# Optimization experiments

Hardware: AMD Instinct MI355X
Metric: run time of the kernel (lower is better)

The kernel has to match this reference:

```python
import jax, jax.numpy as jnp
import numpy as np

# ---- static config (mirrors Net.__init__) ----
N_NODES, N_EDGES = 4000, 20000
N_PROTS, D = 919, 512            # node_emb: Embedding(919, 512); F_in = D (divide_input=False)
TOWERS, F_OUT = 4, D // 4        # F_out = out_channels // towers = 128
EDGE_D = 50
N_GRAPHS, N_CLASSES = 32, 10
N_LAYERS = 2
EPS_BN, EPS_STD = 1e-5, 1e-5

# deg histogram passed to PNAConv; only avg_deg['log'] matters for the scalers used
DEG_HIST = np.array([0., 800., 1200., 900., 600., 300., 150., 50.])
AVG_DEG_LOG = float((np.log(np.arange(DEG_HIST.size) + 1.0) * DEG_HIST).sum() / DEG_HIST.sum())


def setup_inputs() -> dict:
    key = jax.random.key(0)
    ks = jax.random.split(key, 16)
    g = lambda i, shape, s=0.05: (jax.random.normal(ks[i], shape, jnp.float32) * s)
    return dict(
        node_emb_w=g(0, (N_PROTS, D), 0.1),
        edge_emb_w=g(1, (2, EDGE_D), 0.1),
        pe_w=g(2, (2, D)), pe_b=jnp.zeros((D,), jnp.float32),
        edge_enc_w=g(3, (N_LAYERS, EDGE_D, D)), edge_enc_b=jnp.zeros((N_LAYERS, D), jnp.float32),
        pre_w=g(4, (N_LAYERS, TOWERS, 3 * D, D)), pre_b=jnp.zeros((N_LAYERS, TOWERS, D), jnp.float32),
        post_w=g(5, (N_LAYERS, TOWERS, 13 * D, F_OUT)), post_b=jnp.zeros((N_LAYERS, TOWERS, F_OUT), jnp.float32),
        lin_w=g(6, (N_LAYERS, D, D)), lin_b=jnp.zeros((N_LAYERS, D), jnp.float32),
        bn_gamma=jnp.ones((N_LAYERS, D), jnp.float32), bn_beta=jnp.zeros((N_LAYERS, D), jnp.float32),
        acts=jax.random.normal(ks[7], (N_NODES, 2), jnp.float32),
        fc1_w=g(8, (D, 2 * D)), fc1_b=jnp.zeros((2 * D,), jnp.float32),
        fc_out_w=g(9, (2 * D, N_CLASSES)), fc_out_b=jnp.zeros((N_CLASSES,), jnp.float32),
        prelu_a=jnp.float32(0.25),
        global_idx=jax.random.randint(ks[10], (N_NODES,), 0, N_PROTS),
        sign=jax.random.randint(ks[11], (N_EDGES,), 0, 2),
        edge_index=jax.random.randint(ks[12], (2, N_EDGES), 0, N_NODES),
        batch=jnp.sort(jax.random.randint(ks[13], (N_NODES,), 0, N_GRAPHS)),
    )


def _pna_layer(x, src, dst, e, pre_w, pre_b, post_w, post_b, lin_w, lin_b):
    # x: [N, D], e: [E, D] (edge_encoder output), pre_w: [T, 3D, D], post_w: [T, 13D, F_OUT]
    N, E = x.shape[0], src.shape[0]
    # pre-NN on cat([x_i, x_j, edge_attr]) expressed as split matmuls (pre_layers=1 -> single Linear)
    Wi, Wj, We = pre_w[:, :D], pre_w[:, D:2 * D], pre_w[:, 2 * D:]
    m = (jnp.einsum('ef,tfd->etd', x[dst], Wi)
         + jnp.einsum('ef,tfd->etd', x[src], Wj)
         + jnp.einsum('ef,tfd->etd', e, We) + pre_b)          # [E, T, D]
    # multi-aggregation at destination nodes: mean / min / max / std
    cnt = jax.ops.segment_sum(jnp.ones((E,), m.dtype), dst, N)  # in-degree
    has = (cnt > 0)[:, None, None]
    deg = jnp.maximum(cnt, 1.0)[:, None, None]                  # clamp(1) as in PyG
    s1 = jax.ops.segment_sum(m, dst, N)
    s2 = jax.ops.segment_sum(m * m, dst, N)
    mean = s1 / deg
    std = jnp.sqrt(jax.nn.relu(s2 / deg - mean * mean) + EPS_STD)
    mn = jnp.where(has, jax.ops.segment_min(m, dst, N), 0.0)
    mx = jnp.where(has, jax.ops.segment_max(m, dst, N), 0.0)
    agg = jnp.concatenate([mean, mn, mx, std], axis=-1)         # [N, T, 4D]
    # degree scalers: identity, amplification, attenuation
    amp = jnp.log(deg + 1.0) / AVG_DEG_LOG
    out = jnp.concatenate([agg, agg * amp, agg / amp], axis=-1)  # [N, T, 12D]
    # post-NN on cat([x, out]) as split matmuls (post_layers=1)
    Wx, Wo = post_w[:, :D], post_w[:, D:]
    o = (jnp.einsum('nf,tfd->ntd', x, Wx)
         + jnp.einsum('ntf,tfd->ntd', out, Wo) + post_b)        # [N, T, F_OUT]
    return o.reshape(N, TOWERS * F_OUT) @ lin_w + lin_b         # [N, D]


def reference(node_emb_w, edge_emb_w, pe_w, pe_b, edge_enc_w, edge_enc_b,
              pre_w, pre_b, post_w, post_b, lin_w, lin_b, bn_gamma, bn_beta,
              acts, fc1_w, fc1_b, fc_out_w, fc_out_b, prelu_a,
              global_idx, sign, edge_index, batch):
    src, dst = edge_index[0], edge_index[1]
    x = node_emb_w[global_idx] + (acts @ pe_w + pe_b)           # node_emb + PostEncoding
    ea = edge_emb_w[sign]                                       # [E, 50]
    for l in range(N_LAYERS):
        e = ea @ edge_enc_w[l] + edge_enc_b[l]                  # shared edge encoder
        h = _pna_layer(x, src, dst, e, pre_w[l], pre_b[l], post_w[l], post_b[l], lin_w[l], lin_b[l])
        mu = h.mean(axis=0)
        var = ((h - mu) ** 2).mean(axis=0)                      # training-mode BatchNorm (biased var)
        x = jax.nn.relu(bn_gamma[l] * (h - mu) * jax.lax.rsqrt(var + EPS_BN) + bn_beta[l])
    pooled = jax.ops.segment_sum(x, batch, N_GRAPHS)            # global_add_pool
    z = pooled @ fc1_w + fc1_b
    z = jnp.where(z > 0, z, prelu_a * z)                        # PReLU
    logits = z @ fc_out_w + fc_out_b
    return jax.nn.log_softmax(logits, axis=-1)
```

## Files before the change

### kernel.cpp

```cpp
#include <hip/hip_runtime.h>
#include <hip/hip_bf16.h>
#include <float.h>

#define NN 4000
#define NE 20000
#define DD 512
#define NT 4
#define FO 128
#define NG 32
#define NC 10
#define XGW 4608
#define AVGLOG 1.2548916493836102f
#define EPS_STD_ 1e-5f
#define EPS_BN_ 1e-5f

typedef __bf16 bf16x8 __attribute__((ext_vector_type(8)));
typedef float  f32x4  __attribute__((ext_vector_type(4)));

__device__ __forceinline__ void async_copy16(const void* g, void* l) {
    __builtin_amdgcn_global_load_lds((const __attribute__((address_space(1))) void*)g,
                                     (__attribute__((address_space(3))) void*)l, 16, 0, 0);
}

__device__ __forceinline__ void mfma_core128(
    const __bf16* __restrict__ A, int lda,
    const __bf16* __restrict__ BT, int ldbt,
    __bf16* __restrict__ C, int ldc,
    int M, int K, int m0, int n0)
{
    __shared__ __bf16 As[128 * 32];
    __shared__ __bf16 Bs[128 * 32];
    const int tid = threadIdx.x;
    const int wave = tid >> 6, lane = tid & 63;
    const int wm = (wave >> 1) * 64, wn = (wave & 1) * 64;
    const int fr = lane & 15, fq = lane >> 4;
    const int fk = fq * 8;
    const int srow = lane >> 2;
    const int skc = (lane & 3) * 8;

    f32x4 acc[4][4];
    const f32x4 zero = {0.f, 0.f, 0.f, 0.f};
#pragma unroll
    for (int i = 0; i < 4; ++i)
#pragma unroll
        for (int j = 0; j < 4; ++j) acc[i][j] = zero;

    for (int k0 = 0; k0 < K; k0 += 32) {
#pragma unroll
        for (int q = 0; q < 2; ++q) {
            const int row = wave * 32 + q * 16 + srow;
            int ar = m0 + row; if (ar > M - 1) ar = M - 1;
            async_copy16(A + (size_t)ar * lda + k0 + skc, As + wave * 1024 + q * 512);
            async_copy16(BT + (size_t)(n0 + row) * ldbt + k0 + skc, Bs + wave * 1024 + q * 512);
        }
        __syncthreads();
        bf16x8 af[4], bfr[4];
#pragma unroll
        for (int mi = 0; mi < 4; ++mi) af[mi]  = *(const bf16x8*)(As + (wm + mi * 16 + fr) * 32 + fk);
#pragma unroll
        for (int ni = 0; ni < 4; ++ni) bfr[ni] = *(const bf16x8*)(Bs + (wn + ni * 16 + fr) * 32 + fk);
#pragma unroll
        for (int mi = 0; mi < 4; ++mi)
#pragma unroll
            for (int ni = 0; ni < 4; ++ni)
                acc[mi][ni] = __builtin_amdgcn_mfma_f32_16x16x32_bf16(af[mi], bfr[ni], acc[mi][ni], 0, 0, 0);
        __syncthreads();
    }
#pragma unroll
    for (int mi = 0; mi < 4; ++mi) {
#pragma unroll
        for (int ni = 0; ni < 4; ++ni) {
            const int col = n0 + wn + ni * 16 + fr;
            const int rb = m0 + wm + mi * 16 + fq * 4;
#pragma unroll
            for (int r = 0; r < 4; ++r) {
                const int rowc = rb + r;
                if (rowc < M) C[(size_t)rowc * ldc + col] = (__bf16)acc[mi][ni][r];
            }
        }
    }
}

__global__ __launch_bounds__(256) void k_xg(const __bf16* __restrict__ XB, const __bf16* __restrict__ WCAT,
                                            __bf16* __restrict__ XG) {
    mfma_core128(XB, 512, WCAT, 512, XG, XGW, NN, 512, blockIdx.y * 128, blockIdx.x * 128);
}

__global__ __launch_bounds__(256) void k_gw(const __bf16* __restrict__ AB, const __bf16* __restrict__ WTT,
                                            const __bf16* __restrict__ XG,
                                            const float* __restrict__ amp, const float* __restrict__ ramp,
                                            const float* __restrict__ pb, __bf16* __restrict__ OB,
                                            float* __restrict__ BN, float* __restrict__ PL, int zero_pl) {
    const int t = blockIdx.y;
    const int n0 = blockIdx.x * 32;
    __shared__ __bf16 As[32 * 32];
    __shared__ __bf16 Bs[384 * 32];
    __shared__ float  Ep[32][388];
    const int tid = threadIdx.x;
    const int wave = tid >> 6, lane = tid & 63;
    const int fr = lane & 15, fq = lane >> 4;
    const int wn = wave * 96;

    f32x4 acc[2][6];
    const f32x4 zero = {0.f, 0.f, 0.f, 0.f};
#pragma unroll
    for (int i = 0; i < 2; ++i)
#pragma unroll
        for (int j = 0; j < 6; ++j) acc[i][j] = zero;

    const __bf16* Abase = AB + (size_t)n0 * 8192 + (size_t)t * 2048;
    const __bf16* Bbase = WTT + (size_t)t * 384 * 2048;
    const int ar = tid >> 2, akc = (tid & 3) * 8;

    for (int k0 = 0; k0 < 2048; k0 += 32) {
        if (wave < 2)
            async_copy16(Abase + (size_t)ar * 8192 + k0 + akc, As + tid * 8);
#pragma unroll
        for (int i = 0; i < 6; ++i) {
            const int cb = tid + 256 * i;
            const int br = cb >> 2, bkc = (cb & 3) * 8;
            async_copy16(Bbase + (size_t)br * 2048 + k0 + bkc, Bs + cb * 8);
        }
        __syncthreads();
        bf16x8 a[2], b[6];
#pragma unroll
        for (int mi = 0; mi < 2; ++mi) a[mi] = *(const bf16x8*)(As + (mi * 16 + fr) * 32 + fq * 8);
#pragma unroll
        for (int ni = 0; ni < 6; ++ni) b[ni] = *(const bf16x8*)(Bs + (wn + ni * 16 + fr) * 32 + fq * 8);
#pragma unroll
        for (int mi = 0; mi < 2; ++mi)
#pragma unroll
            for (int ni = 0; ni < 6; ++ni)
                acc[mi][ni] = __builtin_amdgcn_mfma_f32_16x16x32_bf16(a[mi], b[ni], acc[mi][ni], 0, 0, 0);
        __syncthreads();
    }
#pragma unroll
    for (int mi = 0; mi < 2; ++mi)
#pragma unroll
        for (int ni = 0; ni < 6; ++ni)
#pragma unroll
            for (int r = 0; r < 4; ++r)
                Ep[mi * 16 + fq * 4 + r][wn + ni * 16 + fr] = acc[mi][ni][r];
    __syncthreads();
    const int row = tid >> 3, o0 = (tid & 7) * 16;
    const int n = n0 + row;
    const float av = amp[n], rv = ramp[n];
    bf16x8 gx0 = *(const bf16x8*)(XG + (size_t)n * XGW + 4096 + t * 128 + o0);
    bf16x8 gx1 = *(const bf16x8*)(XG + (size_t)n * XGW + 4096 + t * 128 + o0 + 8);
    bf16x8 ov0, ov1;
#pragma unroll
    for (int u = 0; u < 8; ++u) {
        int o = o0 + u;
        float v = (float)gx0[u] + Ep[row][o] + av * Ep[row][128 + o] + rv * Ep[row][256 + o] + pb[t * 128 + o];
        ov0[u] = (__bf16)v;
    }
#pragma unroll
    for (int u = 0; u < 8; ++u) {
        int o = o0 + 8 + u;
        float v = (float)gx1[u] + Ep[row][o] + av * Ep[row][128 + o] + rv * Ep[row][256 + o] + pb[t * 128 + o];
        ov1[u] = (__bf16)v;
    }
    *(bf16x8*)(OB + (size_t)n * 512 + t * 128 + o0) = ov0;
    *(bf16x8*)(OB + (size_t)n * 512 + t * 128 + o0 + 8) = ov1;
    if (blockIdx.x == 0 && blockIdx.y == 0) {
        BN[tid] = 0.f; BN[256 + tid] = 0.f; BN[512 + tid] = 0.f; BN[768 + tid] = 0.f;
        if (zero_pl)
            for (int i = tid; i < NG * DD; i += 256) PL[i] = 0.f;
    }
}

__global__ __launch_bounds__(256) void k_lin(const __bf16* __restrict__ OB, const __bf16* __restrict__ WLINT,
                                             const float* __restrict__ bl, float* __restrict__ H,
                                             float* __restrict__ BN) {
    const int n0c = blockIdx.x * 128, m0 = blockIdx.y * 64;
    __shared__ __bf16 As[64 * 32];
    __shared__ __bf16 Bs[128 * 32];
    __shared__ float bnS[128], bnQ[128];
    const int tid = threadIdx.x;
    if (tid < 128) { bnS[tid] = 0.f; bnQ[tid] = 0.f; }
    const int wave = tid >> 6, lane = tid & 63;
    const int wr = wave >> 1, wc = wave & 1;
    const int fr = lane & 15, fq = lane >> 4;
    f32x4 acc[2][4];
    const f32x4 zero = {0.f, 0.f, 0.f, 0.f};
#pragma unroll
    for (int i = 0; i < 2; ++i)
#pragma unroll
        for (int j = 0; j < 4; ++j) acc[i][j] = zero;

    const int ar = tid >> 2, akc = (tid & 3) * 8;
    int arow = m0 + ar; if (arow > NN - 1) arow = NN - 1;
    for (int k0 = 0; k0 < 512; k0 += 32) {
        async_copy16(OB + (size_t)arow * 512 + k0 + akc, As + tid * 8);
#pragma unroll
        for (int i = 0; i < 2; ++i) {
            const int cb = tid + 256 * i;
            const int br = cb >> 2, bkc = (cb & 3) * 8;
            async_copy16(WLINT + (size_t)(n0c + br) * 512 + k0 + bkc, Bs + cb * 8);
        }
        __syncthreads();
        bf16x8 a[2], b[4];
#pragma unroll
        for (int mi = 0; mi < 2; ++mi) a[mi] = *(const bf16x8*)(As + (wr * 32 + mi * 16 + fr) * 32 + fq * 8);
#pragma unroll
        for (int ni = 0; ni < 4; ++ni) b[ni] = *(const bf16x8*)(Bs + (wc * 64 + ni * 16 + fr) * 32 + fq * 8);
#pragma unroll
        for (int mi = 0; mi < 2; ++mi)
#pragma unroll
            for (int ni = 0; ni < 4; ++ni)
                acc[mi][ni] = __builtin_amdgcn_mfma_f32_16x16x32_bf16(a[mi], b[ni], acc[mi][ni], 0, 0, 0);
        __syncthreads();
    }
#pragma unroll
    for (int ni = 0; ni < 4; ++ni) {
        const int lc = wc * 64 + ni * 16 + fr;
        const int col = n0c + lc;
        const float bv = bl[col];
        float s = 0.f, q = 0.f;
#pragma unroll
        for (int mi = 0; mi < 2; ++mi) {
#pragma unroll
            for (int r = 0; r < 4; ++r) {
                const int rowc = m0 + wr * 32 + mi * 16 + fq * 4 + r;
                if (rowc < NN) {
                    const float v = acc[mi][ni][r] + bv;
                    H[(size_t)rowc * 512 + col] = v;
                    s += v; q += v * v;
                }
            }
        }
        atomicAdd(&bnS[lc], s); atomicAdd(&bnQ[lc], q);
    }
    __syncthreads();
    if (tid < 128) {
        atomicAdd(&BN[n0c + tid], bnS[tid]);
        atomicAdd(&BN[512 + n0c + tid], bnQ[tid]);
    }
}

__device__ __forceinline__ void tr32(const float* __restrict__ S, int sld,
                                     __bf16* __restrict__ D, int dld) {
    __shared__ float t[32][33];
    const int x = threadIdx.x, y0 = threadIdx.y * 4;
#pragma unroll
    for (int i = 0; i < 4; ++i) t[y0 + i][x] = S[(size_t)(y0 + i) * sld + x];
    __syncthreads();
#pragma unroll
    for (int i = 0; i < 4; ++i) D[(size_t)(y0 + i) * dld + x] = (__bf16)t[x][y0 + i];
}

__global__ void k_tr(const float* __restrict__ pw, const float* __restrict__ pow_,
                     const float* __restrict__ lw,
                     __bf16* __restrict__ WCAT, __bf16* __restrict__ WTT, __bf16* __restrict__ WLINT) {
    int id = blockIdx.x;
    if (id < 2048) {
        const int z = id >> 8, r = id & 255;
        const int t = z & 3, half = z >> 2;
        const int x = r & 15, y = r >> 4;
        const float* S = pw + ((size_t)(t * 1536 + half * 512 + y * 32)) * 512 + x * 32;
        __bf16* D = WCAT + ((size_t)(half * 2048 + t * 512 + x * 32)) * 512 + y * 32;
        tr32(S, 512, D, 512);
    } else if (id < 2304) {
        const int id3 = id - 2048;
        const int t = id3 >> 6, r = id3 & 63;
        const int x = r & 3, y = r >> 2;
        const float* S = pow_ + ((size_t)(t * 6656 + y * 32)) * 128 + x * 32;
        __bf16* D = WCAT + ((size_t)(4096 + t * 128 + x * 32)) * 512 + y * 32;
        tr32(S, 128, D, 512);
    } else if (id < 5376) {
        const int id4 = id - 2304;
        const int z = id4 >> 8, r = id4 & 255;
        const int t = z / 3, w = z % 3;
        const int x = r & 3, y = r >> 2;
        const float* S = pow_ + ((size_t)(t * 6656 + 512 + w * 2048 + y * 32)) * 128 + x * 32;
        __bf16* D = WTT + (size_t)t * 384 * 2048 + ((size_t)(w * 128 + x * 32)) * 2048 + y * 32;
        tr32(S, 128, D, 2048);
    } else {
        const int r = id - 5376;
        const int x = r & 15, y = r >> 4;
        const float* S = lw + (size_t)y * 32 * 512 + x * 32;
        __bf16* D = WLINT + (size_t)x * 32 * 512 + y * 32;
        tr32(S, 512, D, 512);
    }
}

__global__ void k_count(const int* __restrict__ dst, int* __restrict__ cnt) {
    int e = blockIdx.x * 256 + threadIdx.x;
    if (e < NE) atomicAdd(&cnt[dst[e]], 1);
}

__global__ __launch_bounds__(1024) void k_scan_bx(const int* __restrict__ cnt, int* __restrict__ offs,
                                                  float* __restrict__ amp, float* __restrict__ ramp,
                                                  const float* __restrict__ nemb, const float* __restrict__ acts,
                                                  const float* __restrict__ pew, const float* __restrict__ peb,
                                                  const int* __restrict__ gidx, __bf16* __restrict__ XB) {
    const int t = threadIdx.x;
    if (blockIdx.x == 0) {
        __shared__ int part[1024];
        const int base = t * 4;
        int loc[4]; int s = 0;
#pragma unroll
        for (int i = 0; i < 4; ++i) { int v = (base + i < NN) ? cnt[base + i] : 0; loc[i] = s; s += v; }
        part[t] = s;
        __syncthreads();
        for (int o = 1; o < 1024; o <<= 1) {
            int v = (t >= o) ? part[t - o] : 0;
            __syncthreads();
            part[t] += v;
            __syncthreads();
        }
        const int pre = (t > 0) ? part[t - 1] : 0;
#pragma unroll
        for (int i = 0; i < 4; ++i) if (base + i < NN) offs[base + i] = pre + loc[i];
        if (t == 1023) offs[NN] = part[1023];
        for (int n = t; n < NN; n += 1024) {
            float deg = fmaxf((float)cnt[n], 1.0f);
            float a = logf(deg + 1.0f) / AVGLOG;
            amp[n] = a; ramp[n] = 1.0f / a;
        }
    } else {
        const int idx = (blockIdx.x - 1) * 1024 + t;
        const int n = idx >> 9, d = idx & 511;
        float v = nemb[(size_t)gidx[n] * DD + d] + acts[n * 2] * pew[d] + acts[n * 2 + 1] * pew[DD + d] + peb[d];
        XB[idx] = (__bf16)v;
    }
}

__global__ void k_fill(const int* __restrict__ src, const int* __restrict__ dst,
                       const int* __restrict__ sgn, const int* __restrict__ offs,
                       int* __restrict__ fill, int* __restrict__ esrc, int* __restrict__ esgn) {
    int e = blockIdx.x * 256 + threadIdx.x;
    if (e < NE) {
        int d = dst[e];
        int pos = offs[d] + atomicAdd(&fill[d], 1);
        esrc[pos] = src[e];
        esgn[pos] = sgn[e];
    }
}

__global__ __launch_bounds__(256) void k_em(const float* __restrict__ eemb, const float* __restrict__ eew,
                                            const float* __restrict__ eeb, const float* __restrict__ pw,
                                            const float* __restrict__ pb, float* __restrict__ EM) {
    __shared__ float eks[512];
    __shared__ float part[4][64];
    const int tid = threadIdx.x;
    const int k = blockIdx.x >> 5;
    const int g0 = (blockIdx.x & 31) * 64;
#pragma unroll
    for (int h = 0; h < 2; ++h) {
        const int f = tid + h * 256;
        float s = eeb[f];
        for (int c = 0; c < 50; ++c) s += eemb[k * 50 + c] * eew[(size_t)c * 512 + f];
        eks[f] = s;
    }
    __syncthreads();
    const int wave = tid >> 6, lane = tid & 63;
    const int g = g0 + lane;
    const int t = g >> 9, d = g & 511;
    const float* Wp = pw + ((size_t)(t * 1536 + 1024)) * 512 + d;
    float s = 0.f;
    const int f0 = wave * 128;
#pragma unroll 4
    for (int f = f0; f < f0 + 128; ++f) s += eks[f] * Wp[(size_t)f * 512];
    part[wave][lane] = s;
    __syncthreads();
    if (tid < 64) {
        const int gg = g0 + tid;
        EM[k * 2048 + gg] = pb[gg] + part[0][tid] + part[1][tid] + part[2][tid] + part[3][tid];
    }
}

__global__ __launch_bounds__(256) void k_agg(const __bf16* __restrict__ XG, const float* __restrict__ EM,
                                             const int* __restrict__ offs, const int* __restrict__ cnt,
                                             const int* __restrict__ esrc, const int* __restrict__ esgn,
                                             __bf16* __restrict__ AB) {
    const int n = blockIdx.x;
    const int g = threadIdx.x * 8;
    float xid[8], em0[8], em1[8];
    {
        bf16x8 xb = *(const bf16x8*)(XG + (size_t)n * XGW + g);
#pragma unroll
        for (int i = 0; i < 8; ++i) xid[i] = (float)xb[i];
    }
    *(float4*)&em0[0] = *(const float4*)&EM[g];
    *(float4*)&em0[4] = *(const float4*)&EM[g + 4];
    *(float4*)&em1[0] = *(const float4*)&EM[2048 + g];
    *(float4*)&em1[4] = *(const float4*)&EM[2048 + g + 4];
    float s1[8], s2[8], mn[8], mx[8];
#pragma unroll
    for (int i = 0; i < 8; ++i) { s1[i] = 0.f; s2[i] = 0.f; mn[i] = FLT_MAX; mx[i] = -FLT_MAX; }
    const int j0 = offs[n], j1 = offs[n + 1];
    for (int j = j0; j < j1; ++j) {
        const int s = esrc[j];
        const int sg = esgn[j];
        bf16x8 xv = *(const bf16x8*)(XG + (size_t)s * XGW + 2048 + g);
#pragma unroll
        for (int i = 0; i < 8; ++i) {
            float m = xid[i] + (float)xv[i] + (sg ? em1[i] : em0[i]);
            s1[i] += m; s2[i] += m * m;
            mn[i] = fminf(mn[i], m); mx[i] = fmaxf(mx[i], m);
        }
    }
    const int c = cnt[n];
    const float deg = fmaxf((float)c, 1.0f);
    const float rdeg = 1.0f / deg;
    bf16x8 vmean, vmn, vmx, vsd;
#pragma unroll
    for (int i = 0; i < 8; ++i) {
        float mean = s1[i] * rdeg;
        float var = s2[i] * rdeg - mean * mean;
        float sd = sqrtf(fmaxf(var, 0.f) + EPS_STD_);
        float mnv = (c == 0) ? 0.f : mn[i];
        float mxv = (c == 0) ? 0.f : mx[i];
        vmean[i] = (__bf16)mean; vmn[i] = (__bf16)mnv; vmx[i] = (__bf16)mxv; vsd[i] = (__bf16)sd;
    }
    const int t = g >> 9, d = g & 511;
    __bf16* base = AB + (size_t)n * 8192 + (size_t)t * 2048 + d;
    *(bf16x8*)(base + 0 * DD) = vmean;
    *(bf16x8*)(base + 1 * DD) = vmn;
    *(bf16x8*)(base + 2 * DD) = vmx;
    *(bf16x8*)(base + 3 * DD) = vsd;
}

__global__ void k_bnapply(const float* __restrict__ H, const float* __restrict__ BN,
                          const float* __restrict__ gamma, const float* __restrict__ beta,
                          __bf16* __restrict__ XB, float* __restrict__ PL,
                          const int* __restrict__ batch, int last) {
    int idx = blockIdx.x * 256 + threadIdx.x;
    int n = idx >> 9, d = idx & 511;
    float mu = BN[d] * (1.0f / NN);
    float var = BN[512 + d] * (1.0f / NN) - mu * mu;
    float v = gamma[d] * (H[idx] - mu) * rsqrtf(var + EPS_BN_) + beta[d];
    v = fmaxf(v, 0.f);
    if (last) atomicAdd(&PL[(size_t)batch[n] * DD + d], v);
    else XB[idx] = (__bf16)v;
}

__global__ __launch_bounds__(256) void k_head(const float* __restrict__ PL, const float* __restrict__ W1,
                                              const float* __restrict__ b1, const float* __restrict__ Wo,
                                              const float* __restrict__ bo, const float* __restrict__ pa,
                                              float* __restrict__ out) {
    __shared__ float pl[512];
    __shared__ float zz[1024];
    __shared__ float lgs[NC];
    const int g = blockIdx.x, tid = threadIdx.x;
    pl[tid] = PL[(size_t)g * 512 + tid];
    pl[tid + 256] = PL[(size_t)g * 512 + 256 + tid];
    if (tid < NC) lgs[tid] = bo[tid];
    __syncthreads();
    const float a = *pa;
#pragma unroll
    for (int h = 0; h < 4; ++h) {
        const int j = tid + h * 256;
        float s0 = 0.f, s1 = 0.f, s2 = 0.f, s3 = 0.f;
        for (int f = 0; f < 512; f += 4) {
            s0 += pl[f + 0] * W1[(size_t)(f + 0) * 1024 + j];
            s1 += pl[f + 1] * W1[(size_t)(f + 1) * 1024 + j];
            s2 += pl[f + 2] * W1[(size_t)(f + 2) * 1024 + j];
            s3 += pl[f + 3] * W1[(size_t)(f + 3) * 1024 + j];
        }
        float s = b1[j] + ((s0 + s1) + (s2 + s3));
        zz[j] = s > 0.f ? s : a * s;
    }
    __syncthreads();
    float p[NC];
#pragma unroll
    for (int c = 0; c < NC; ++c) p[c] = 0.f;
    for (int f = tid; f < 1024; f += 256) {
        const float z = zz[f];
#pragma unroll
        for (int c = 0; c < NC; ++c) p[c] += z * Wo[(size_t)f * NC + c];
    }
#pragma unroll
    for (int off = 32; off > 0; off >>= 1)
#pragma unroll
        for (int c = 0; c < NC; ++c) p[c] += __shfl_down(p[c], off);
    if ((tid & 63) == 0)
#pragma unroll
        for (int c = 0; c < NC; ++c) atomicAdd(&lgs[c], p[c]);
    __syncthreads();
    if (tid == 0) {
        float mxv = -FLT_MAX;
#pragma unroll
        for (int c = 0; c < NC; ++c) mxv = fmaxf(mxv, lgs[c]);
        float se = 0.f;
#pragma unroll
        for (int c = 0; c < NC; ++c) se += expf(lgs[c] - mxv);
        const float lse = mxv + logf(se);
#pragma unroll
        for (int c = 0; c < NC; ++c) out[g * NC + c] = lgs[c] - lse;
    }
}

extern "C" void kernel_launch(void* const* d_in, const int* in_sizes, int n_in,
                              void* d_out, int out_size, void* d_ws, size_t ws_size,
                              hipStream_t stream) {
    const float* node_emb_w = (const float*)d_in[0];
    const float* edge_emb_w = (const float*)d_in[1];
    const float* pe_w   = (const float*)d_in[2];
    const float* pe_b   = (const float*)d_in[3];
    const float* edge_enc_w = (const float*)d_in[4];
    const float* edge_enc_b = (const float*)d_in[5];
    const float* pre_w  = (const float*)d_in[6];
    const float* pre_b  = (const float*)d_in[7];
    const float* post_w = (const float*)d_in[8];
    const float* post_b = (const float*)d_in[9];
    const float* lin_w  = (const float*)d_in[10];
    const float* lin_b  = (const float*)d_in[11];
    const float* bn_gamma = (const float*)d_in[12];
    const float* bn_beta  = (const float*)d_in[13];
    const float* acts   = (const float*)d_in[14];
    const float* fc1_w  = (const float*)d_in[15];
    const float* fc1_b  = (const float*)d_in[16];
    const float* fc_out_w = (const float*)d_in[17];
    const float* fc_out_b = (const float*)d_in[18];
    const float* prelu_a  = (const float*)d_in[19];
    const int* global_idx = (const int*)d_in[20];
    const int* sgn        = (const int*)d_in[21];
    const int* edge_index = (const int*)d_in[22];
    const int* batch      = (const int*)d_in[23];
    float* out = (float*)d_out;

    char* W = (char*)d_ws;
    size_t off = 0;
    auto alloc = [&](size_t bytes) { void* p = W + off; off += (bytes + 63) & ~(size_t)63; return p; };
    __bf16* XB    = (__bf16*)alloc((size_t)NN * DD * 2);
    float*  H     = (float*)alloc((size_t)NN * DD * 4);
    __bf16* XG    = (__bf16*)alloc((size_t)NN * XGW * 2);
    __bf16* AB    = (__bf16*)alloc((size_t)NN * 8192 * 2);
    __bf16* OB    = (__bf16*)alloc((size_t)NN * DD * 2);
    __bf16* WCAT  = (__bf16*)alloc((size_t)XGW * 512 * 2);
    __bf16* WTT   = (__bf16*)alloc((size_t)NT * 384 * 2048 * 2);
    __bf16* WLINT = (__bf16*)alloc((size_t)512 * 512 * 2);
    float*  EM    = (float*)alloc(2 * 2048 * 4);
    float*  BN    = (float*)alloc(1024 * 4);
    float*  PL    = (float*)alloc((size_t)NG * DD * 4);
    float*  AMP   = (float*)alloc(NN * 4);
    float*  RAMP  = (float*)alloc(NN * 4);
    int*    CNT   = (int*)alloc(NN * 4);
    int*    FILL  = (int*)alloc(NN * 4);
    int*    OFFS  = (int*)alloc((NN + 1) * 4);
    int*    ESRC  = (int*)alloc(NE * 4);
    int*    ESGN  = (int*)alloc(NE * 4);

    const int* src = edge_index;
    const int* dst = edge_index + NE;

    hipMemsetAsync(CNT, 0, 2 * NN * sizeof(int), stream);
    k_count<<<(NE + 255) / 256, 256, 0, stream>>>(dst, CNT);
    k_scan_bx<<<2001, 1024, 0, stream>>>(CNT, OFFS, AMP, RAMP,
                                         node_emb_w, acts, pe_w, pe_b, global_idx, XB);
    k_fill<<<(NE + 255) / 256, 256, 0, stream>>>(src, dst, sgn, OFFS, FILL, ESRC, ESGN);

    for (int l = 0; l < 2; ++l) {
        const float* pre_w_l  = pre_w  + (size_t)l * NT * 3 * DD * DD;
        const float* pre_b_l  = pre_b  + (size_t)l * NT * DD;
        const float* post_w_l = post_w + (size_t)l * NT * 6656 * FO;
        const float* post_b_l = post_b + (size_t)l * NT * FO;
        const float* lin_w_l  = lin_w  + (size_t)l * DD * DD;
        const float* lin_b_l  = lin_b  + (size_t)l * DD;
        const float* eew_l    = edge_enc_w + (size_t)l * 50 * DD;
        const float* eeb_l    = edge_enc_b + (size_t)l * DD;

        k_tr<<<5632, dim3(32, 8), 0, stream>>>(pre_w_l, post_w_l, lin_w_l, WCAT, WTT, WLINT);
        k_em<<<64, 256, 0, stream>>>(edge_emb_w, eew_l, eeb_l, pre_w_l, pre_b_l, EM);
        k_xg<<<dim3(36, 32), 256, 0, stream>>>(XB, WCAT, XG);
        k_agg<<<NN, 256, 0, stream>>>(XG, EM, OFFS, CNT, ESRC, ESGN, AB);
        k_gw<<<dim3(125, 4), 256, 0, stream>>>(AB, WTT, XG, AMP, RAMP, post_b_l, OB, BN, PL, l == 1);
        k_lin<<<dim3(4, 63), 256, 0, stream>>>(OB, WLINT, lin_b_l, H, BN);
        k_bnapply<<<NN * DD / 256, 256, 0, stream>>>(H, BN, bn_gamma + (size_t)l * DD,
                                                     bn_beta + (size_t)l * DD, XB, PL, batch, l == 1);
    }

    k_head<<<NG, 256, 0, stream>>>(PL, fc1_w, fc1_b, fc_out_w, fc_out_b, prelu_a, out);
}
```

Before: 582.2 us.

## Split-K the post-tower GEMM and shrink GEMM tiles for more parallelism

The tower post-GEMM becomes a split-K (two halves) generic 64x128-tile GEMM writing fp32 partials. A new elementwise kernel sums the partials, applies the amplification/attenuation scalers, bias and residual XG term, and zeroes BN/PL. The XG GEMM also moves from 128x128 to 64x128 tiles. The goal is more blocks and better CU occupancy on small-M GEMMs, at the cost of a large fp32 partial buffer (~49MB) written and reread, plus an extra launch.

```diff
diff --git a/kernel.cpp b/kernel.cpp
--- a/kernel.cpp
+++ b/kernel.cpp
@@ -22,60 +22,66 @@
                                      (__attribute__((address_space(3))) void*)l, 16, 0, 0);
 }
 
-__device__ __forceinline__ void mfma_core128(
+template<int OUT_BF16, int HAS_BIAS>
+__device__ __forceinline__ void core64(
     const __bf16* __restrict__ A, int lda,
     const __bf16* __restrict__ BT, int ldbt,
-    __bf16* __restrict__ C, int ldc,
+    void* __restrict__ Cv, int ldc,
+    const float* __restrict__ bias,
     int M, int K, int m0, int n0)
 {
-    __shared__ __bf16 As[128 * 32];
+    __shared__ __bf16 As[64 * 32];
     __shared__ __bf16 Bs[128 * 32];
     const int tid = threadIdx.x;
     const int wave = tid >> 6, lane = tid & 63;
-    const int wm = (wave >> 1) * 64, wn = (wave & 1) * 64;
+    const int wr = wave >> 1, wc = wave & 1;
     const int fr = lane & 15, fq = lane >> 4;
-    const int fk = fq * 8;
-    const int srow = lane >> 2;
-    const int skc = (lane & 3) * 8;
-
-    f32x4 acc[4][4];
+    f32x4 acc[2][4];
     const f32x4 zero = {0.f, 0.f, 0.f, 0.f};
 #pragma unroll
-    for (int i = 0; i < 4; ++i)
+    for (int i = 0; i < 2; ++i)
 #pragma unroll
         for (int j = 0; j < 4; ++j) acc[i][j] = zero;
 
+    const int ar = tid >> 2, akc = (tid & 3) * 8;
+    int arow = m0 + ar; if (arow > M - 1) arow = M - 1;
     for (int k0 = 0; k0 < K; k0 += 32) {
-#pragma unroll
-        for (int q = 0; q < 2; ++q) {
-            const int row = wave * 32 + q * 16 + srow;
-            int ar = m0 + row; if (ar > M - 1) ar = M - 1;
-            async_copy16(A + (size_t)ar * lda + k0 + skc, As + wave * 1024 + q * 512);
-            async_copy16(BT + (size_t)(n0 + row) * ldbt + k0 + skc, Bs + wave * 1024 + q * 512);
+        async_copy16(A + (size_t)arow * lda + k0 + akc, As + tid * 8);
+#pragma unroll
+        for (int i = 0; i < 2; ++i) {
+            const int cb = tid + 256 * i;
+            const int br = cb >> 2, bkc = (cb & 3) * 8;
+            async_copy16(BT + (size_t)(n0 + br) * ldbt + k0 + bkc, Bs + cb * 8);
         }
         __syncthreads();
-        bf16x8 af[4], bfr[4];
-#pragma unroll
-        for (int mi = 0; mi < 4; ++mi) af[mi]  = *(const bf16x8*)(As + (wm + mi * 16 + fr) * 32 + fk);
-#pragma unroll
-        for (int ni = 0; ni < 4; ++ni) bfr[ni] = *(const bf16x8*)(Bs + (wn + ni * 16 + fr) * 32 + fk);
-#pragma unroll
-        for (int mi = 0; mi < 4; ++mi)
+        bf16x8 a[2], b[4];
+#pragma unroll
+        for (int mi = 0; mi < 2; ++mi) a[mi] = *(const bf16x8*)(As + (wr * 32 + mi * 16 + fr) * 32 + fq * 8);
+#pragma unroll
+        for (int ni = 0; ni < 4; ++ni) b[ni] = *(const bf16x8*)(Bs + (wc * 64 + ni * 16 + fr) * 32 + fq * 8);
+#pragma unroll
+        for (int mi = 0; mi < 2; ++mi)
 #pragma unroll
             for (int ni = 0; ni < 4; ++ni)
-                acc[mi][ni] = __builtin_amdgcn_mfma_f32_16x16x32_bf16(af[mi], bfr[ni], acc[mi][ni], 0, 0, 0);
+                acc[mi][ni] = __builtin_amdgcn_mfma_f32_16x16x32_bf16(a[mi], b[ni], acc[mi][ni], 0, 0, 0);
         __syncthreads();
     }
-#pragma unroll
-    for (int mi = 0; mi < 4; ++mi) {
+    float* Cf = (float*)Cv; __bf16* Cb = (__bf16*)Cv;
+#pragma unroll
+    for (int mi = 0; mi < 2; ++mi) {
 #pragma unroll
         for (int ni = 0; ni < 4; ++ni) {
-            const int col = n0 + wn + ni * 16 + fr;
-            const int rb = m0 + wm + mi * 16 + fq * 4;
+            const int col = n0 + wc * 64 + ni * 16 + fr;
+            const int rb = m0 + wr * 32 + mi * 16 + fq * 4;
+            const float bv = HAS_BIAS ? bias[col] : 0.f;
 #pragma unroll
             for (int r = 0; r < 4; ++r) {
                 const int rowc = rb + r;
-                if (rowc < M) C[(size_t)rowc * ldc + col] = (__bf16)acc[mi][ni][r];
+                if (rowc < M) {
+                    const float v = acc[mi][ni][r] + bv;
+                    if (OUT_BF16) Cb[(size_t)rowc * ldc + col] = (__bf16)v;
+                    else          Cf[(size_t)rowc * ldc + col] = v;
+                }
             }
         }
     }
@@ -83,86 +89,37 @@
 
 __global__ __launch_bounds__(256) void k_xg(const __bf16* __restrict__ XB, const __bf16* __restrict__ WCAT,
                                             __bf16* __restrict__ XG) {
-    mfma_core128(XB, 512, WCAT, 512, XG, XGW, NN, 512, blockIdx.y * 128, blockIdx.x * 128);
+    core64<1, 0>(XB, 512, WCAT, 512, XG, XGW, nullptr, NN, 512,
+                 blockIdx.y * 64, blockIdx.x * 128);
 }
 
 __global__ __launch_bounds__(256) void k_gw(const __bf16* __restrict__ AB, const __bf16* __restrict__ WTT,
-                                            const __bf16* __restrict__ XG,
-                                            const float* __restrict__ amp, const float* __restrict__ ramp,
-                                            const float* __restrict__ pb, __bf16* __restrict__ OB,
-                                            float* __restrict__ BN, float* __restrict__ PL, int zero_pl) {
-    const int t = blockIdx.y;
-    const int n0 = blockIdx.x * 32;
-    __shared__ __bf16 As[32 * 32];
-    __shared__ __bf16 Bs[384 * 32];
-    __shared__ float  Ep[32][388];
-    const int tid = threadIdx.x;
-    const int wave = tid >> 6, lane = tid & 63;
-    const int fr = lane & 15, fq = lane >> 4;
-    const int wn = wave * 96;
-
-    f32x4 acc[2][6];
-    const f32x4 zero = {0.f, 0.f, 0.f, 0.f};
-#pragma unroll
-    for (int i = 0; i < 2; ++i)
-#pragma unroll
-        for (int j = 0; j < 6; ++j) acc[i][j] = zero;
-
-    const __bf16* Abase = AB + (size_t)n0 * 8192 + (size_t)t * 2048;
-    const __bf16* Bbase = WTT + (size_t)t * 384 * 2048;
-    const int ar = tid >> 2, akc = (tid & 3) * 8;
-
-    for (int k0 = 0; k0 < 2048; k0 += 32) {
-        if (wave < 2)
-            async_copy16(Abase + (size_t)ar * 8192 + k0 + akc, As + tid * 8);
-#pragma unroll
-        for (int i = 0; i < 6; ++i) {
-            const int cb = tid + 256 * i;
-            const int br = cb >> 2, bkc = (cb & 3) * 8;
-            async_copy16(Bbase + (size_t)br * 2048 + k0 + bkc, Bs + cb * 8);
-        }
-        __syncthreads();
-        bf16x8 a[2], b[6];
-#pragma unroll
-        for (int mi = 0; mi < 2; ++mi) a[mi] = *(const bf16x8*)(As + (mi * 16 + fr) * 32 + fq * 8);
-#pragma unroll
-        for (int ni = 0; ni < 6; ++ni) b[ni] = *(const bf16x8*)(Bs + (wn + ni * 16 + fr) * 32 + fq * 8);
-#pragma unroll
-        for (int mi = 0; mi < 2; ++mi)
-#pragma unroll
-            for (int ni = 0; ni < 6; ++ni)
-                acc[mi][ni] = __builtin_amdgcn_mfma_f32_16x16x32_bf16(a[mi], b[ni], acc[mi][ni], 0, 0, 0);
-        __syncthreads();
-    }
-#pragma unroll
-    for (int mi = 0; mi < 2; ++mi)
-#pragma unroll
-        for (int ni = 0; ni < 6; ++ni)
-#pragma unroll
-            for (int r = 0; r < 4; ++r)
-                Ep[mi * 16 + fq * 4 + r][wn + ni * 16 + fr] = acc[mi][ni][r];
-    __syncthreads();
-    const int row = tid >> 3, o0 = (tid & 7) * 16;
-    const int n = n0 + row;
-    const float av = amp[n], rv = ramp[n];
-    bf16x8 gx0 = *(const bf16x8*)(XG + (size_t)n * XGW + 4096 + t * 128 + o0);
-    bf16x8 gx1 = *(const bf16x8*)(XG + (size_t)n * XGW + 4096 + t * 128 + o0 + 8);
-    bf16x8 ov0, ov1;
-#pragma unroll
-    for (int u = 0; u < 8; ++u) {
-        int o = o0 + u;
-        float v = (float)gx0[u] + Ep[row][o] + av * Ep[row][128 + o] + rv * Ep[row][256 + o] + pb[t * 128 + o];
-        ov0[u] = (__bf16)v;
-    }
-#pragma unroll
-    for (int u = 0; u < 8; ++u) {
-        int o = o0 + 8 + u;
-        float v = (float)gx1[u] + Ep[row][o] + av * Ep[row][128 + o] + rv * Ep[row][256 + o] + pb[t * 128 + o];
-        ov1[u] = (__bf16)v;
-    }
-    *(bf16x8*)(OB + (size_t)n * 512 + t * 128 + o0) = ov0;
-    *(bf16x8*)(OB + (size_t)n * 512 + t * 128 + o0 + 8) = ov1;
-    if (blockIdx.x == 0 && blockIdx.y == 0) {
+                                            float* __restrict__ GWP) {
+    const int t = blockIdx.z & 3, kh = blockIdx.z >> 2;
+    const __bf16* A  = AB  + (size_t)t * 2048 + (size_t)kh * 1024;
+    const __bf16* BT = WTT + (size_t)t * 384 * 2048 + (size_t)kh * 1024;
+    float* C = GWP + (size_t)blockIdx.z * NN * 384;
+    core64<0, 0>(A, 8192, BT, 2048, C, 384, nullptr, NN, 1024,
+                 blockIdx.y * 64, blockIdx.x * 128);
+}
+
+__global__ void k_combine(const __bf16* __restrict__ XG, const float* __restrict__ GWP,
+                          const float* __restrict__ amp, const float* __restrict__ ramp,
+                          const float* __restrict__ pb, __bf16* __restrict__ OB,
+                          float* __restrict__ BN, float* __restrict__ PL, int zero_pl) {
+    const int idx = blockIdx.x * 256 + threadIdx.x;
+    const int n = idx >> 9, c = idx & 511;
+    const int t = c >> 7, o = c & 127;
+    const float* ga = GWP + ((size_t)t) * NN * 384 + (size_t)n * 384;
+    const float* gb = GWP + ((size_t)(4 + t)) * NN * 384 + (size_t)n * 384;
+    const float w1 = ga[o] + gb[o];
+    const float w2 = ga[128 + o] + gb[128 + o];
+    const float w3 = ga[256 + o] + gb[256 + o];
+    const float gx = (float)XG[(size_t)n * XGW + 4096 + c];
+    const float v = gx + w1 + amp[n] * w2 + ramp[n] * w3 + pb[c];
+    OB[idx] = (__bf16)v;
+    if (blockIdx.x == 0) {
+        const int tid = threadIdx.x;
         BN[tid] = 0.f; BN[256 + tid] = 0.f; BN[512 + tid] = 0.f; BN[768 + tid] = 0.f;
         if (zero_pl)
             for (int i = tid; i < NG * DD; i += 256) PL[i] = 0.f;
@@ -528,6 +485,7 @@
     float*  H     = (float*)alloc((size_t)NN * DD * 4);
     __bf16* XG    = (__bf16*)alloc((size_t)NN * XGW * 2);
     __bf16* AB    = (__bf16*)alloc((size_t)NN * 8192 * 2);
+    float*  GWP   = (float*)alloc((size_t)8 * NN * 384 * 4);
     __bf16* OB    = (__bf16*)alloc((size_t)NN * DD * 2);
     __bf16* WCAT  = (__bf16*)alloc((size_t)XGW * 512 * 2);
     __bf16* WTT   = (__bf16*)alloc((size_t)NT * 384 * 2048 * 2);
@@ -564,9 +522,10 @@
 
         k_tr<<<5632, dim3(32, 8), 0, stream>>>(pre_w_l, post_w_l, lin_w_l, WCAT, WTT, WLINT);
         k_em<<<64, 256, 0, stream>>>(edge_emb_w, eew_l, eeb_l, pre_w_l, pre_b_l, EM);
-        k_xg<<<dim3(36, 32), 256, 0, stream>>>(XB, WCAT, XG);
+        k_xg<<<dim3(36, 63), 256, 0, stream>>>(XB, WCAT, XG);
         k_agg<<<NN, 256, 0, stream>>>(XG, EM, OFFS, CNT, ESRC, ESGN, AB);
-        k_gw<<<dim3(125, 4), 256, 0, stream>>>(AB, WTT, XG, AMP, RAMP, post_b_l, OB, BN, PL, l == 1);
+        k_gw<<<dim3(3, 63, 8), 256, 0, stream>>>(AB, WTT, GWP);
+        k_combine<<<NN * DD / 256, 256, 0, stream>>>(XG, GWP, AMP, RAMP, post_b_l, OB, BN, PL, l == 1);
         k_lin<<<dim3(4, 63), 256, 0, stream>>>(OB, WLINT, lin_b_l, H, BN);
         k_bnapply<<<NN * DD / 256, 256, 0, stream>>>(H, BN, bn_gamma + (size_t)l * DD,
                                                      bn_beta + (size_t)l * DD, XB, PL, batch, l == 1);
```

New measurement: 589.8 us. No clear change (+1.3%).
